# Kernel tuning notes

Measured on AMD Instinct MI355X. Metric: run time of the kernel, lower is better.

Reference implementation:

```python
import jax, jax.numpy as jnp
import numpy as np

B, N, C, H = 32, 577, 768, 12
D = C // H  # head_dim = 64


def _rotate_half(t):
    half = t.shape[-1] // 2
    return jnp.concatenate([-t[..., half:], t[..., :half]], axis=-1)


def _rope(t, sin, cos):
    # t: [B, H, N-1, D]; sin/cos: [N-1, D] broadcast over batch and heads
    return t * cos + _rotate_half(t) * sin


def setup_inputs() -> dict:
    key = jax.random.key(0)
    ks = jax.random.split(key, 5)
    x = jax.random.normal(ks[0], (B, N, C), dtype=jnp.float32)
    w_qkv = jax.random.normal(ks[1], (C, 3 * C), dtype=jnp.float32) * (1.0 / np.sqrt(C))
    b_qkv = jnp.zeros((3 * C,), dtype=jnp.float32)
    w_proj = jax.random.normal(ks[2], (C, C), dtype=jnp.float32) * (1.0 / np.sqrt(C))
    b_proj = jnp.zeros((C,), dtype=jnp.float32)
    # rotary tables for the N-1 non-CLS tokens
    pos = jnp.arange(N - 1, dtype=jnp.float32)[:, None]            # [N-1, 1]
    inv_freq = 1.0 / (10000.0 ** (jnp.arange(0, D, 2, dtype=jnp.float32) / D))  # [D/2]
    ang = pos * inv_freq[None, :]                                   # [N-1, D/2]
    ang = jnp.concatenate([ang, ang], axis=-1)                      # [N-1, D]
    rope_sin = jnp.sin(ang)
    rope_cos = jnp.cos(ang)
    return {"x": x, "w_qkv": w_qkv, "b_qkv": b_qkv, "w_proj": w_proj,
            "b_proj": b_proj, "rope_sin": rope_sin, "rope_cos": rope_cos}


def reference(x, w_qkv, b_qkv, w_proj, b_proj, rope_sin, rope_cos):
    Bx, Nx, Cx = x.shape
    qkv = x @ w_qkv + b_qkv                                   # [B, N, 3C]
    qkv = qkv.reshape(Bx, Nx, 3, H, D).transpose(2, 0, 3, 1, 4)  # [3, B, H, N, D]
    q, k, v = qkv[0], qkv[1], qkv[2]
    # RoPE only on non-CLS tokens (index 0 is CLS)
    q = jnp.concatenate([q[:, :, :1, :], _rope(q[:, :, 1:, :], rope_sin, rope_cos)], axis=2)
    k = jnp.concatenate([k[:, :, :1, :], _rope(k[:, :, 1:, :], rope_sin, rope_cos)], axis=2)
    q = q / jnp.sqrt(jnp.float32(D))
    attn = jnp.einsum("bhqd,bhkd->bhqk", q, k)               # [B, H, N, N]
    attn = jax.nn.softmax(attn.astype(jnp.float32), axis=-1).astype(x.dtype)
    out = jnp.einsum("bhqk,bhkd->bhqd", attn, v)             # [B, H, N, D]
    out = out.transpose(0, 2, 1, 3).reshape(Bx, Nx, Cx)       # [B, N, C]
    return out @ w_proj + b_proj
```

## Files before the change

kernel.cpp:

```cpp
#include <hip/hip_runtime.h>

#define Bdim 32
#define Ndim 577
#define Cdim 768
#define Hdim 12
#define Ddim 64
#define Mdim (Bdim*Ndim)
#define VSTRIDE 640
#define TSTRIDE 152
#define QSCALE 0.18033688f
#define MGRP 19

typedef __attribute__((ext_vector_type(4))) float f32x4;
typedef __attribute__((ext_vector_type(8))) __bf16 bf16x8;
typedef __attribute__((ext_vector_type(4))) __bf16 bf16x4;

__device__ __forceinline__ void gl_lds16(const __bf16* g, __bf16* l) {
  __builtin_amdgcn_global_load_lds((const __attribute__((address_space(1))) void*)g,
                                   (__attribute__((address_space(3))) void*)l, 16, 0, 0);
}

__global__ __launch_bounds__(256) void f32_to_bf16(const float4* __restrict__ in,
                                                   bf16x4* __restrict__ out, int n4) {
  int i = blockIdx.x * 256 + threadIdx.x;
  if (i < n4) {
    float4 v = in[i];
    bf16x4 o = {(__bf16)v.x, (__bf16)v.y, (__bf16)v.z, (__bf16)v.w};
    out[i] = o;
  }
}

__global__ __launch_bounds__(256) void transpose_f32_wfrag(const float* __restrict__ in,
                                                           __bf16* __restrict__ out,
                                                           int Cc) {
  __shared__ float tile[64][65];
  int bx = blockIdx.x * 64;
  int by = blockIdx.y * 64;
  int tx = threadIdx.x & 63, ty = threadIdx.x >> 6;
  #pragma unroll
  for (int i = ty; i < 64; i += 4)
    tile[i][tx] = in[(size_t)(by + i) * Cc + bx + tx];
  __syncthreads();
  #pragma unroll
  for (int it = 0; it < 2; ++it) {
    int idx = it * 256 + threadIdx.x;
    int nl = idx & 63, kc = idx >> 6;
    bf16x8 o;
    #pragma unroll
    for (int j = 0; j < 8; ++j) o[j] = (__bf16)tile[kc * 8 + j][nl];
    int n = bx + nl, kk = by + kc * 8;
    *(bf16x8*)(out + ((size_t)(n >> 4) * 96 + (kk >> 3)) * 128 + (n & 15) * 8) = o;
  }
}

__device__ __forceinline__ void gemm_split_core(const __bf16* __restrict__ A,
                                                const __bf16* __restrict__ WF,
                                                int m0, int n0,
                                                __bf16* As, f32x4 acc[4][4]) {
  const int t = threadIdx.x;
  const int lane = t & 63, w = t >> 6;
  const int quad = lane >> 4, l16 = lane & 15;
  const int wm = w >> 1, wn = w & 1;
  const int nb16 = (n0 >> 4) + wn * 4;

  for (int k0 = 0; k0 < 768; k0 += 64) {
    __syncthreads();
    bf16x8 b[2][4];
    #pragma unroll
    for (int s = 0; s < 2; ++s)
      #pragma unroll
      for (int i = 0; i < 4; ++i)
        b[s][i] = *(const bf16x8*)(WF +
            ((size_t)(nb16 + i) * 96 + (k0 >> 3) + s * 4 + quad) * 128 + l16 * 8);
    #pragma unroll
    for (int e = 0; e < 4; ++e) {
      int h = e >> 1;
      int j = ((e & 1) << 2) | w;
      int row = j * 16 + (lane >> 2);
      int col = k0 + h * 32 + (lane & 3) * 8;
      int ar = m0 + row; if (ar > Mdim - 1) ar = Mdim - 1;
      gl_lds16(A + (size_t)ar * 768 + col, As + h * 4096 + j * 512 + lane * 8);
    }
    __syncthreads();
    #pragma unroll
    for (int s = 0; s < 2; ++s) {
      bf16x8 a[4];
      #pragma unroll
      for (int i = 0; i < 4; ++i)
        a[i] = *(const bf16x8*)(As + s * 4096 + (wm * 64 + i * 16 + l16) * 32 + quad * 8);
      #pragma unroll
      for (int mt = 0; mt < 4; ++mt)
        #pragma unroll
        for (int nt = 0; nt < 4; ++nt)
          acc[mt][nt] = __builtin_amdgcn_mfma_f32_16x16x32_bf16(a[mt], b[s][nt], acc[mt][nt], 0, 0, 0);
    }
  }
}

__device__ __forceinline__ bool xcd_decode(int lin, int nb, int mb, int& n, int& m) {
  int x8 = lin & 7;
  int rest = lin >> 3;
  n = rest % nb;
  int mg = rest / nb;
  m = mg * 8 + x8;
  return m < mb;
}

__global__ __launch_bounds__(256) void qk_kernel(const __bf16* __restrict__ x,
                                                 const __bf16* __restrict__ wf,
                                                 const float* __restrict__ b_qkv,
                                                 const float* __restrict__ rs,
                                                 const float* __restrict__ rc,
                                                 __bf16* __restrict__ q,
                                                 __bf16* __restrict__ k) {
  __shared__ __bf16 As[2 * 128 * 32];
  int nb, mbk;
  if (!xcd_decode(blockIdx.x, 12, 145, nb, mbk)) return;
  const int n0 = nb * 128, m0 = mbk * 128;

  f32x4 acc[4][4];
  const f32x4 fz = {0.f, 0.f, 0.f, 0.f};
  for (int i = 0; i < 4; ++i) for (int j = 0; j < 4; ++j) acc[i][j] = fz;
  gemm_split_core(x, wf, m0, n0, As, acc);

  const int lane = threadIdx.x & 63, w = threadIdx.x >> 6;
  const int quad = lane >> 4, l16 = lane & 15;
  const int wm = w >> 1, wn = w & 1;
  const int colbase = n0 + wn * 64;
  const int matrix = colbase / 768;
  const int head = (colbase % 768) / 64;

  #pragma unroll
  for (int mt = 0; mt < 4; ++mt) {
    int mbase = m0 + wm * 64 + mt * 16 + quad * 4;
    #pragma unroll
    for (int r = 0; r < 4; ++r) {
      int m = mbase + r;
      if (m >= Mdim) continue;
      int bb = m / 577, tok = m % 577;
      #pragma unroll
      for (int nt = 0; nt < 4; ++nt) {
        int d = nt * 16 + l16;
        float val = acc[mt][nt][r] + b_qkv[colbase + d];
        if (tok > 0) {
          float partner = acc[mt][nt ^ 2][r] + b_qkv[colbase + (d ^ 32)];
          float sn = rs[(size_t)(tok - 1) * 64 + d];
          float cs = rc[(size_t)(tok - 1) * 64 + d];
          float rot = (d < 32) ? -partner : partner;
          val = val * cs + rot * sn;
        }
        __bf16* dst;
        if (matrix == 0) { val *= QSCALE; dst = q; } else dst = k;
        dst[((size_t)(bb * 12 + head) * 577 + tok) * 64 + d] = (__bf16)val;
      }
    }
  }
}

__global__ __launch_bounds__(256) void v_kernel(const __bf16* __restrict__ x,
                                                const __bf16* __restrict__ wf,
                                                const float* __restrict__ b_qkv,
                                                __bf16* __restrict__ vt) {
  __shared__ __bf16 As[2 * 128 * 32];
  __shared__ __bf16 Ts[64 * TSTRIDE];
  int nb, mbk;
  if (!xcd_decode(blockIdx.x, 6, 145, nb, mbk)) return;
  const int n0 = 1536 + nb * 128, m0 = mbk * 128;

  f32x4 acc[4][4];
  const f32x4 fz = {0.f, 0.f, 0.f, 0.f};
  for (int i = 0; i < 4; ++i) for (int j = 0; j < 4; ++j) acc[i][j] = fz;
  gemm_split_core(x, wf, m0, n0, As, acc);

  const int t = threadIdx.x;
  const int lane = t & 63, w = t >> 6;
  const int quad = lane >> 4, l16 = lane & 15;
  const int wm = w >> 1, wn = w & 1;
  const int colbase = n0 + wn * 64;

  #pragma unroll
  for (int h = 0; h < 2; ++h) {
    __syncthreads();
    if (wn == h) {
      #pragma unroll
      for (int mt = 0; mt < 4; ++mt) {
        int tokbase = wm * 64 + mt * 16 + quad * 4;
        #pragma unroll
        for (int r = 0; r < 4; ++r) {
          #pragma unroll
          for (int nt = 0; nt < 4; ++nt) {
            int dl = nt * 16 + l16;
            Ts[dl * TSTRIDE + tokbase + r] =
                (__bf16)(acc[mt][nt][r] + b_qkv[colbase + dl]);
          }
        }
      }
    }
    __syncthreads();
    int hh = (n0 + h * 64 - 1536) / 64;
    #pragma unroll
    for (int it = 0; it < 4; ++it) {
      int c = it * 256 + t;
      int dl = c >> 4, chunk = c & 15;
      bf16x8 vv = *(const bf16x8*)(Ts + dl * TSTRIDE + chunk * 8);
      #pragma unroll
      for (int j = 0; j < 8; ++j) {
        int m = m0 + chunk * 8 + j;
        if (m < Mdim) {
          int bb = m / 577, tok = m % 577;
          vt[((size_t)(bb * 12 + hh) * 64 + dl) * VSTRIDE + tok] = vv[j];
        }
      }
    }
  }
}

__global__ __launch_bounds__(256) void attn_kernel(const __bf16* __restrict__ q,
                                                   const __bf16* __restrict__ k,
                                                   const __bf16* __restrict__ vt,
                                                   __bf16* __restrict__ ao) {
  __shared__ __bf16 qs[4096];
  __shared__ __bf16 ks[4096];
  __shared__ __bf16 vs[4096];
  __shared__ __bf16 ps[64 * 72];

  const int x8 = blockIdx.x & 7;
  const int rest = blockIdx.x >> 3;
  const int qt = rest % 10;
  const int bh = (rest / 10) * 8 + x8;

  const int t = threadIdx.x;
  const int lane = t & 63, w = t >> 6;
  const int quad = lane >> 4, l16 = lane & 15;

  const __bf16* qbase = q + (size_t)bh * 577 * 64;
  const __bf16* kbase = k + (size_t)bh * 577 * 64;
  const __bf16* vbase = vt + (size_t)bh * 64 * VSTRIDE;

  #pragma unroll
  for (int p = 0; p < 2; ++p) {
    int g = p * 256 + t;
    int d8 = g >> 6, tok = g & 63;
    gl_lds16(qbase + (size_t)(qt * 64 + tok) * 64 + d8 * 8, qs + (size_t)g * 8);
  }

  bf16x8 kreg[2], vreg[2];
  #pragma unroll
  for (int p = 0; p < 2; ++p) {
    int g = p * 256 + t;
    kreg[p] = *(const bf16x8*)(kbase + (size_t)(g & 63) * 64 + (g >> 6) * 8);
    vreg[p] = *(const bf16x8*)(vbase + (size_t)(g & 63) * VSTRIDE + (g >> 6) * 8);
  }

  f32x4 O[4]; const f32x4 fz = {0.f, 0.f, 0.f, 0.f};
  for (int i = 0; i < 4; ++i) O[i] = fz;
  float l_part[4] = {0.f, 0.f, 0.f, 0.f};

  for (int kt = 0; kt < 10; ++kt) {
    __syncthreads();
    #pragma unroll
    for (int p = 0; p < 2; ++p) {
      int g = p * 256 + t;
      *(bf16x8*)(ks + (size_t)g * 8) = kreg[p];
      *(bf16x8*)(vs + (size_t)g * 8) = vreg[p];
    }
    __syncthreads();

    if (kt < 9) {
      #pragma unroll
      for (int p = 0; p < 2; ++p) {
        int g = p * 256 + t;
        kreg[p] = *(const bf16x8*)(kbase + (size_t)((kt + 1) * 64 + (g & 63)) * 64 + (g >> 6) * 8);
        vreg[p] = *(const bf16x8*)(vbase + (size_t)(g & 63) * VSTRIDE + (kt + 1) * 64 + (g >> 6) * 8);
      }
      __builtin_amdgcn_sched_barrier(0);
    }

    f32x4 S[4]; for (int i = 0; i < 4; ++i) S[i] = fz;
    __builtin_amdgcn_s_setprio(1);
    #pragma unroll
    for (int step = 0; step < 2; ++step) {
      bf16x8 a = *(const bf16x8*)(qs + (size_t)((step * 4 + quad) * 64 + w * 16 + l16) * 8);
      #pragma unroll
      for (int nt = 0; nt < 4; ++nt) {
        bf16x8 b = *(const bf16x8*)(ks + (size_t)((step * 4 + quad) * 64 + nt * 16 + l16) * 8);
        S[nt] = __builtin_amdgcn_mfma_f32_16x16x32_bf16(a, b, S[nt], 0, 0, 0);
      }
    }
    __builtin_amdgcn_s_setprio(0);

    int kv_left = 577 - kt * 64;
    if (kv_left < 64) {
      #pragma unroll
      for (int nt = 0; nt < 4; ++nt) {
        int c = nt * 16 + l16;
        if (c >= kv_left) { S[nt][0] = -1e30f; S[nt][1] = -1e30f; S[nt][2] = -1e30f; S[nt][3] = -1e30f; }
      }
    }

    #pragma unroll
    for (int r = 0; r < 4; ++r) {
      #pragma unroll
      for (int nt = 0; nt < 4; ++nt) {
        float e = exp2f(S[nt][r]);
        l_part[r] += e;
        ps[(size_t)(w * 16 + quad * 4 + r) * 72 + nt * 16 + l16] = (__bf16)e;
      }
    }

    __builtin_amdgcn_s_setprio(1);
    #pragma unroll
    for (int step = 0; step < 2; ++step) {
      bf16x8 a = *(const bf16x8*)(ps + (size_t)(w * 16 + l16) * 72 + step * 32 + quad * 8);
      #pragma unroll
      for (int dt = 0; dt < 4; ++dt) {
        bf16x8 b = *(const bf16x8*)(vs + (size_t)((step * 4 + quad) * 64 + dt * 16 + l16) * 8);
        O[dt] = __builtin_amdgcn_mfma_f32_16x16x32_bf16(a, b, O[dt], 0, 0, 0);
      }
    }
    __builtin_amdgcn_s_setprio(0);
  }

  const int bb = bh / 12, hh = bh % 12;
  const int qrow0 = qt * 64 + w * 16 + quad * 4;
  #pragma unroll
  for (int r = 0; r < 4; ++r) {
    float l = l_part[r];
    l += __shfl_xor(l, 1); l += __shfl_xor(l, 2);
    l += __shfl_xor(l, 4); l += __shfl_xor(l, 8);
    int row = qrow0 + r;
    if (row < 577) {
      float inv = 1.f / l;
      size_t base = ((size_t)(bb * 577 + row)) * 768 + hh * 64;
      #pragma unroll
      for (int dt = 0; dt < 4; ++dt)
        ao[base + dt * 16 + l16] = (__bf16)(O[dt][r] * inv);
    }
  }
}

__global__ __launch_bounds__(256) void proj_kernel(const __bf16* __restrict__ ao,
                                                   const __bf16* __restrict__ wprojF,
                                                   const float* __restrict__ b_proj,
                                                   float* __restrict__ out) {
  __shared__ __bf16 As[2 * 128 * 32];
  int nb, mbk;
  if (!xcd_decode(blockIdx.x, 6, 145, nb, mbk)) return;
  const int n0 = nb * 128, m0 = mbk * 128;

  f32x4 acc[4][4];
  const f32x4 fz = {0.f, 0.f, 0.f, 0.f};
  for (int i = 0; i < 4; ++i) for (int j = 0; j < 4; ++j) acc[i][j] = fz;
  gemm_split_core(ao, wprojF, m0, n0, As, acc);

  const int lane = threadIdx.x & 63, w = threadIdx.x >> 6;
  const int quad = lane >> 4, l16 = lane & 15;
  const int wm = w >> 1, wn = w & 1;
  const int colbase = n0 + wn * 64;

  #pragma unroll
  for (int mt = 0; mt < 4; ++mt) {
    int mbase = m0 + wm * 64 + mt * 16 + quad * 4;
    #pragma unroll
    for (int r = 0; r < 4; ++r) {
      int m = mbase + r;
      if (m >= Mdim) continue;
      #pragma unroll
      for (int nt = 0; nt < 4; ++nt) {
        int c = colbase + nt * 16 + l16;
        out[(size_t)m * 768 + c] = acc[mt][nt][r] + b_proj[c];
      }
    }
  }
}

extern "C" void kernel_launch(void* const* d_in, const int* in_sizes, int n_in,
                              void* d_out, int out_size, void* d_ws, size_t ws_size,
                              hipStream_t stream) {
  const float* x      = (const float*)d_in[0];
  const float* w_qkv  = (const float*)d_in[1];
  const float* b_qkv  = (const float*)d_in[2];
  const float* w_proj = (const float*)d_in[3];
  const float* b_proj = (const float*)d_in[4];
  const float* rsn    = (const float*)d_in[5];
  const float* rcs    = (const float*)d_in[6];
  float* out = (float*)d_out;

  constexpr size_t QK_E = (size_t)Bdim * Hdim * Ndim * Ddim;
  constexpr size_t VT_E = (size_t)Bdim * Hdim * Ddim * VSTRIDE;
  constexpr size_t AO_E = (size_t)Mdim * Cdim;
  __bf16* q      = (__bf16*)d_ws;
  __bf16* k      = q + QK_E;
  __bf16* vt     = k + QK_E;
  __bf16* ao     = vt + VT_E;
  __bf16* xb     = ao;
  __bf16* wqkvF  = ao + AO_E;
  __bf16* wprojF = wqkvF + (size_t)2304 * 768;

  f32_to_bf16<<<13848, 256, 0, stream>>>((const float4*)x, (bf16x4*)xb,
                                         (int)(AO_E / 4));
  transpose_f32_wfrag<<<dim3(36, 12), 256, 0, stream>>>(w_qkv, wqkvF, 2304);
  transpose_f32_wfrag<<<dim3(12, 12), 256, 0, stream>>>(w_proj, wprojF, 768);
  qk_kernel<<<8 * MGRP * 12, 256, 0, stream>>>(xb, wqkvF, b_qkv, rsn, rcs, q, k);
  v_kernel<<<8 * MGRP * 6, 256, 0, stream>>>(xb, wqkvF, b_qkv, vt);
  attn_kernel<<<3840, 256, 0, stream>>>(q, k, vt, ao);
  proj_kernel<<<8 * MGRP * 6, 256, 0, stream>>>(ao, wprojF, b_proj, out);
}
```

Baseline: 425.1 us.

## Load attention Q/K/V MFMA operands directly from global memory, dropping LDS staging

The attention kernel no longer stages Q, K and V tiles through shared memory with register prefetch and two block barriers per KV tile. Each wave now keeps its Q fragment in registers and reads its K and V MFMA operands straight from global memory inside the loop. This removes the LDS writes, the __syncthreads and the LDS footprint, which could raise occupancy. In exchange all four waves fetch the same K/V data separately and rely on the caches. The software prefetch of the next tile is also gone, so global load latency sits directly in front of the MFMAs.

```diff
diff --git a/kernel.cpp b/kernel.cpp
--- a/kernel.cpp
+++ b/kernel.cpp
@@ -219,9 +219,6 @@
                                                    const __bf16* __restrict__ k,
                                                    const __bf16* __restrict__ vt,
                                                    __bf16* __restrict__ ao) {
-  __shared__ __bf16 qs[4096];
-  __shared__ __bf16 ks[4096];
-  __shared__ __bf16 vs[4096];
   __shared__ __bf16 ps[64 * 72];
 
   const int x8 = blockIdx.x & 7;
@@ -237,54 +234,25 @@
   const __bf16* kbase = k + (size_t)bh * 577 * 64;
   const __bf16* vbase = vt + (size_t)bh * 64 * VSTRIDE;
 
-  #pragma unroll
-  for (int p = 0; p < 2; ++p) {
-    int g = p * 256 + t;
-    int d8 = g >> 6, tok = g & 63;
-    gl_lds16(qbase + (size_t)(qt * 64 + tok) * 64 + d8 * 8, qs + (size_t)g * 8);
-  }
-
-  bf16x8 kreg[2], vreg[2];
-  #pragma unroll
-  for (int p = 0; p < 2; ++p) {
-    int g = p * 256 + t;
-    kreg[p] = *(const bf16x8*)(kbase + (size_t)(g & 63) * 64 + (g >> 6) * 8);
-    vreg[p] = *(const bf16x8*)(vbase + (size_t)(g & 63) * VSTRIDE + (g >> 6) * 8);
-  }
+  bf16x8 aq[2];
+  #pragma unroll
+  for (int s = 0; s < 2; ++s)
+    aq[s] = *(const bf16x8*)(qbase + (size_t)(qt * 64 + w * 16 + l16) * 64 + (s * 4 + quad) * 8);
 
   f32x4 O[4]; const f32x4 fz = {0.f, 0.f, 0.f, 0.f};
   for (int i = 0; i < 4; ++i) O[i] = fz;
   float l_part[4] = {0.f, 0.f, 0.f, 0.f};
 
   for (int kt = 0; kt < 10; ++kt) {
-    __syncthreads();
-    #pragma unroll
-    for (int p = 0; p < 2; ++p) {
-      int g = p * 256 + t;
-      *(bf16x8*)(ks + (size_t)g * 8) = kreg[p];
-      *(bf16x8*)(vs + (size_t)g * 8) = vreg[p];
-    }
-    __syncthreads();
-
-    if (kt < 9) {
-      #pragma unroll
-      for (int p = 0; p < 2; ++p) {
-        int g = p * 256 + t;
-        kreg[p] = *(const bf16x8*)(kbase + (size_t)((kt + 1) * 64 + (g & 63)) * 64 + (g >> 6) * 8);
-        vreg[p] = *(const bf16x8*)(vbase + (size_t)(g & 63) * VSTRIDE + (kt + 1) * 64 + (g >> 6) * 8);
-      }
-      __builtin_amdgcn_sched_barrier(0);
-    }
-
     f32x4 S[4]; for (int i = 0; i < 4; ++i) S[i] = fz;
     __builtin_amdgcn_s_setprio(1);
     #pragma unroll
-    for (int step = 0; step < 2; ++step) {
-      bf16x8 a = *(const bf16x8*)(qs + (size_t)((step * 4 + quad) * 64 + w * 16 + l16) * 8);
-      #pragma unroll
-      for (int nt = 0; nt < 4; ++nt) {
-        bf16x8 b = *(const bf16x8*)(ks + (size_t)((step * 4 + quad) * 64 + nt * 16 + l16) * 8);
-        S[nt] = __builtin_amdgcn_mfma_f32_16x16x32_bf16(a, b, S[nt], 0, 0, 0);
+    for (int s = 0; s < 2; ++s) {
+      #pragma unroll
+      for (int nt = 0; nt < 4; ++nt) {
+        bf16x8 bk = *(const bf16x8*)(kbase +
+            (size_t)(kt * 64 + nt * 16 + l16) * 64 + (s * 4 + quad) * 8);
+        S[nt] = __builtin_amdgcn_mfma_f32_16x16x32_bf16(aq[s], bk, S[nt], 0, 0, 0);
       }
     }
     __builtin_amdgcn_s_setprio(0);
@@ -310,12 +278,13 @@
 
     __builtin_amdgcn_s_setprio(1);
     #pragma unroll
-    for (int step = 0; step < 2; ++step) {
-      bf16x8 a = *(const bf16x8*)(ps + (size_t)(w * 16 + l16) * 72 + step * 32 + quad * 8);
+    for (int s = 0; s < 2; ++s) {
+      bf16x8 a = *(const bf16x8*)(ps + (size_t)(w * 16 + l16) * 72 + s * 32 + quad * 8);
       #pragma unroll
       for (int dt = 0; dt < 4; ++dt) {
-        bf16x8 b = *(const bf16x8*)(vs + (size_t)((step * 4 + quad) * 64 + dt * 16 + l16) * 8);
-        O[dt] = __builtin_amdgcn_mfma_f32_16x16x32_bf16(a, b, O[dt], 0, 0, 0);
+        bf16x8 bv = *(const bf16x8*)(vbase +
+            (size_t)(dt * 16 + l16) * VSTRIDE + kt * 64 + (s * 4 + quad) * 8);
+        O[dt] = __builtin_amdgcn_mfma_f32_16x16x32_bf16(a, bv, O[dt], 0, 0, 0);
       }
     }
     __builtin_amdgcn_s_setprio(0);
```

New measurement: 608.9 us. 43.3% more time.

## Process two query tiles per attention block to reuse staged K/V tiles

Applied to the files above, without the earlier changes.

Each attention block now covers 128 query rows (two 64-row tiles) instead of 64, so every K/V tile loaded into LDS feeds twice as many QK and PV MFMAs. The grid is halved to match. Q fragments are loaded straight into registers, which drops the Q shared-memory buffer and its async LDS load. In exchange, register pressure rises from the doubled O accumulators and Q fragments, and the smaller grid gives fewer blocks for latency hiding.

```diff
diff --git a/kernel.cpp b/kernel.cpp
--- a/kernel.cpp
+++ b/kernel.cpp
@@ -219,15 +219,14 @@
                                                    const __bf16* __restrict__ k,
                                                    const __bf16* __restrict__ vt,
                                                    __bf16* __restrict__ ao) {
-  __shared__ __bf16 qs[4096];
   __shared__ __bf16 ks[4096];
   __shared__ __bf16 vs[4096];
   __shared__ __bf16 ps[64 * 72];
 
   const int x8 = blockIdx.x & 7;
   const int rest = blockIdx.x >> 3;
-  const int qt = rest % 10;
-  const int bh = (rest / 10) * 8 + x8;
+  const int qp = rest % 5;
+  const int bh = (rest / 5) * 8 + x8;
 
   const int t = threadIdx.x;
   const int lane = t & 63, w = t >> 6;
@@ -237,12 +236,13 @@
   const __bf16* kbase = k + (size_t)bh * 577 * 64;
   const __bf16* vbase = vt + (size_t)bh * 64 * VSTRIDE;
 
-  #pragma unroll
-  for (int p = 0; p < 2; ++p) {
-    int g = p * 256 + t;
-    int d8 = g >> 6, tok = g & 63;
-    gl_lds16(qbase + (size_t)(qt * 64 + tok) * 64 + d8 * 8, qs + (size_t)g * 8);
-  }
+  bf16x8 aq[2][2];
+  #pragma unroll
+  for (int qi = 0; qi < 2; ++qi)
+    #pragma unroll
+    for (int s = 0; s < 2; ++s)
+      aq[qi][s] = *(const bf16x8*)(qbase +
+          (size_t)(qp * 128 + qi * 64 + w * 16 + l16) * 64 + (s * 4 + quad) * 8);
 
   bf16x8 kreg[2], vreg[2];
   #pragma unroll
@@ -252,9 +252,9 @@
     vreg[p] = *(const bf16x8*)(vbase + (size_t)(g & 63) * VSTRIDE + (g >> 6) * 8);
   }
 
-  f32x4 O[4]; const f32x4 fz = {0.f, 0.f, 0.f, 0.f};
-  for (int i = 0; i < 4; ++i) O[i] = fz;
-  float l_part[4] = {0.f, 0.f, 0.f, 0.f};
+  f32x4 O[2][4]; const f32x4 fz = {0.f, 0.f, 0.f, 0.f};
+  for (int qi = 0; qi < 2; ++qi) for (int i = 0; i < 4; ++i) O[qi][i] = fz;
+  float l_part[2][4] = {{0.f, 0.f, 0.f, 0.f}, {0.f, 0.f, 0.f, 0.f}};
 
   for (int kt = 0; kt < 10; ++kt) {
     __syncthreads();
@@ -276,65 +276,71 @@
       __builtin_amdgcn_sched_barrier(0);
     }
 
-    f32x4 S[4]; for (int i = 0; i < 4; ++i) S[i] = fz;
-    __builtin_amdgcn_s_setprio(1);
-    #pragma unroll
-    for (int step = 0; step < 2; ++step) {
-      bf16x8 a = *(const bf16x8*)(qs + (size_t)((step * 4 + quad) * 64 + w * 16 + l16) * 8);
-      #pragma unroll
-      for (int nt = 0; nt < 4; ++nt) {
-        bf16x8 b = *(const bf16x8*)(ks + (size_t)((step * 4 + quad) * 64 + nt * 16 + l16) * 8);
-        S[nt] = __builtin_amdgcn_mfma_f32_16x16x32_bf16(a, b, S[nt], 0, 0, 0);
-      }
-    }
-    __builtin_amdgcn_s_setprio(0);
-
     int kv_left = 577 - kt * 64;
-    if (kv_left < 64) {
-      #pragma unroll
-      for (int nt = 0; nt < 4; ++nt) {
-        int c = nt * 16 + l16;
-        if (c >= kv_left) { S[nt][0] = -1e30f; S[nt][1] = -1e30f; S[nt][2] = -1e30f; S[nt][3] = -1e30f; }
-      }
-    }
-
+
+    #pragma unroll
+    for (int qi = 0; qi < 2; ++qi) {
+      f32x4 S[4]; for (int i = 0; i < 4; ++i) S[i] = fz;
+      __builtin_amdgcn_s_setprio(1);
+      #pragma unroll
+      for (int s = 0; s < 2; ++s) {
+        #pragma unroll
+        for (int nt = 0; nt < 4; ++nt) {
+          bf16x8 b = *(const bf16x8*)(ks + (size_t)((s * 4 + quad) * 64 + nt * 16 + l16) * 8);
+          S[nt] = __builtin_amdgcn_mfma_f32_16x16x32_bf16(aq[qi][s], b, S[nt], 0, 0, 0);
+        }
+      }
+      __builtin_amdgcn_s_setprio(0);
+
+      if (kv_left < 64) {
+        #pragma unroll
+        for (int nt = 0; nt < 4; ++nt) {
+          int c = nt * 16 + l16;
+          if (c >= kv_left) { S[nt][0] = -1e30f; S[nt][1] = -1e30f; S[nt][2] = -1e30f; S[nt][3] = -1e30f; }
+        }
+      }
+
+      #pragma unroll
+      for (int r = 0; r < 4; ++r) {
+        #pragma unroll
+        for (int nt = 0; nt < 4; ++nt) {
+          float e = exp2f(S[nt][r]);
+          l_part[qi][r] += e;
+          ps[(size_t)(w * 16 + quad * 4 + r) * 72 + nt * 16 + l16] = (__bf16)e;
+        }
+      }
+
+      __builtin_amdgcn_s_setprio(1);
+      #pragma unroll
+      for (int s = 0; s < 2; ++s) {
+        bf16x8 a = *(const bf16x8*)(ps + (size_t)(w * 16 + l16) * 72 + s * 32 + quad * 8);
+        #pragma unroll
+        for (int dt = 0; dt < 4; ++dt) {
+          bf16x8 b = *(const bf16x8*)(vs + (size_t)((s * 4 + quad) * 64 + dt * 16 + l16) * 8);
+          O[qi][dt] = __builtin_amdgcn_mfma_f32_16x16x32_bf16(a, b, O[qi][dt], 0, 0, 0);
+        }
+      }
+      __builtin_amdgcn_s_setprio(0);
+    }
+  }
+
+  const int bb = bh / 12, hh = bh % 12;
+  #pragma unroll
+  for (int qi = 0; qi < 2; ++qi) {
+    const int qrow0 = qp * 128 + qi * 64 + w * 16 + quad * 4;
     #pragma unroll
     for (int r = 0; r < 4; ++r) {
-      #pragma unroll
-      for (int nt = 0; nt < 4; ++nt) {
-        float e = exp2f(S[nt][r]);
-        l_part[r] += e;
-        ps[(size_t)(w * 16 + quad * 4 + r) * 72 + nt * 16 + l16] = (__bf16)e;
-      }
-    }
-
-    __builtin_amdgcn_s_setprio(1);
-    #pragma unroll
-    for (int step = 0; step < 2; ++step) {
-      bf16x8 a = *(const bf16x8*)(ps + (size_t)(w * 16 + l16) * 72 + step * 32 + quad * 8);
-      #pragma unroll
-      for (int dt = 0; dt < 4; ++dt) {
-        bf16x8 b = *(const bf16x8*)(vs + (size_t)((step * 4 + quad) * 64 + dt * 16 + l16) * 8);
-        O[dt] = __builtin_amdgcn_mfma_f32_16x16x32_bf16(a, b, O[dt], 0, 0, 0);
-      }
-    }
-    __builtin_amdgcn_s_setprio(0);
-  }
-
-  const int bb = bh / 12, hh = bh % 12;
-  const int qrow0 = qt * 64 + w * 16 + quad * 4;
-  #pragma unroll
-  for (int r = 0; r < 4; ++r) {
-    float l = l_part[r];
-    l += __shfl_xor(l, 1); l += __shfl_xor(l, 2);
-    l += __shfl_xor(l, 4); l += __shfl_xor(l, 8);
-    int row = qrow0 + r;
-    if (row < 577) {
-      float inv = 1.f / l;
-      size_t base = ((size_t)(bb * 577 + row)) * 768 + hh * 64;
-      #pragma unroll
-      for (int dt = 0; dt < 4; ++dt)
-        ao[base + dt * 16 + l16] = (__bf16)(O[dt][r] * inv);
+      float l = l_part[qi][r];
+      l += __shfl_xor(l, 1); l += __shfl_xor(l, 2);
+      l += __shfl_xor(l, 4); l += __shfl_xor(l, 8);
+      int row = qrow0 + r;
+      if (row < 577) {
+        float inv = 1.f / l;
+        size_t base = ((size_t)(bb * 577 + row)) * 768 + hh * 64;
+        #pragma unroll
+        for (int dt = 0; dt < 4; ++dt)
+          ao[base + dt * 16 + l16] = (__bf16)(O[qi][dt][r] * inv);
+      }
     }
   }
 }
@@ -403,6 +409,6 @@
   transpose_f32_wfrag<<<dim3(12, 12), 256, 0, stream>>>(w_proj, wprojF, 768);
   qk_kernel<<<8 * MGRP * 12, 256, 0, stream>>>(xb, wqkvF, b_qkv, rsn, rcs, q, k);
   v_kernel<<<8 * MGRP * 6, 256, 0, stream>>>(xb, wqkvF, b_qkv, vt);
-  attn_kernel<<<3840, 256, 0, stream>>>(q, k, vt, ao);
+  attn_kernel<<<1920, 256, 0, stream>>>(q, k, vt, ao);
   proj_kernel<<<8 * MGRP * 6, 256, 0, stream>>>(ao, wprojF, b_proj, out);
 }
```

Result: no change. 418.9 us (-1.4%).
